# Kernel optimization log

Hardware: AMD Instinct MI355X
Metric: run time of the kernel (lower is better)

Reference implementation:

```python
import math
import jax, jax.numpy as jnp
import numpy as np

B, S, D, L = 8, 4096, 1024, 16

def setup_inputs() -> dict:
    key = jax.random.key(0)
    k1, k2, k3 = jax.random.split(key, 3)
    memory = jax.random.normal(k1, (B, S, D), dtype=jnp.float32)
    summarizer = jax.random.normal(k2, (L, D), dtype=jnp.float32) * 0.02
    w_proj = jax.random.normal(k3, (1, L), dtype=jnp.float32) * (1.0 / math.sqrt(L))
    return {"memory": memory, "summarizer": summarizer, "w_proj": w_proj}

def reference(memory, summarizer, w_proj):
    # scores: [B, L, S] = summarizer @ memory^T / sqrt(D)
    d = summarizer.shape[-1]
    scores = jnp.einsum('ld,bsd->bls', summarizer, memory) / jnp.sqrt(jnp.asarray(d, memory.dtype))
    p_attn = jax.nn.softmax(scores, axis=-1)            # softmax over sequence S
    ctx = jnp.einsum('bls,bsd->bld', p_attn, memory)    # [B, L, D]
    # nn.Linear(L, 1, bias=False) applied to ctx.transpose(-1,-2): [B, D, L] @ W^T -> [B, D, 1]
    out = jnp.einsum('bld,l->bd', ctx, w_proj[0])       # [B, D]
    return out[:, None, :]                              # [B, 1, D] after final transpose
```

## Files before the change

### kernel.cpp

```cpp
#include <hip/hip_runtime.h>
#include <hip/hip_bf16.h>

#define BB 8
#define SS 4096
#define DD 1024
#define LL 16

typedef __attribute__((ext_vector_type(8))) short short8;
typedef __attribute__((ext_vector_type(4))) float fl4;

static __device__ __forceinline__ short f2bf(float f) {
    unsigned u = __float_as_uint(f);
    u += 0x7FFFu + ((u >> 16) & 1u);
    return (short)(u >> 16);
}

__global__ __launch_bounds__(256) void k_prep(const float* __restrict__ summ,
                                              short* __restrict__ summb) {
    int i = blockIdx.x * 256 + threadIdx.x;
    if (i < LL * DD) summb[i] = f2bf(summ[i]);
}

__global__ __launch_bounds__(256) void k_scores(const float* __restrict__ mem,
                                                const short* __restrict__ summb,
                                                float* __restrict__ e) {
    int gwave = (blockIdx.x * 256 + threadIdx.x) >> 6;
    int lane  = threadIdx.x & 63;
    int b     = gwave >> 8;
    int s0    = (gwave & 255) << 4;
    int o  = lane & 15;
    int qd = lane >> 4;

    const short* arow = summb + o * DD + qd * 8;
    const float* mrow = mem + ((size_t)b * SS + (size_t)(s0 + o)) * DD + qd * 8;

    fl4 acc = {0.f, 0.f, 0.f, 0.f};
    #pragma unroll 8
    for (int k = 0; k < DD; k += 32) {
        short8 a = *(const short8*)(arow + k);
        fl4 f0 = *(const fl4*)(mrow + k);
        fl4 f1 = *(const fl4*)(mrow + k + 4);
        short8 bb;
        bb[0] = f2bf(f0[0]); bb[1] = f2bf(f0[1]);
        bb[2] = f2bf(f0[2]); bb[3] = f2bf(f0[3]);
        bb[4] = f2bf(f1[0]); bb[5] = f2bf(f1[1]);
        bb[6] = f2bf(f1[2]); bb[7] = f2bf(f1[3]);
        acc = __builtin_amdgcn_mfma_f32_16x16x32_bf16(a, bb, acc, 0, 0, 0);
    }

    const float scale = 0.03125f;
    float* ebase = e + (size_t)b * LL * SS + s0 + o;
    #pragma unroll
    for (int r = 0; r < 4; ++r) {
        int l = qd * 4 + r;
        ebase[(size_t)l * SS] = __expf(acc[r] * scale);
    }
}

__global__ __launch_bounds__(1024) void k_softmax_q(const float* __restrict__ e,
                                                    const float* __restrict__ w,
                                                    float* __restrict__ qout) {
    int b = blockIdx.x;
    int t = threadIdx.x;
    int l = t >> 6, u = t & 63;
    __shared__ float coef[LL];
    const float* eb = e + (size_t)b * LL * SS;

    float sum = 0.f;
    #pragma unroll 8
    for (int s = u; s < SS; s += 64) sum += eb[(size_t)l * SS + s];
    #pragma unroll
    for (int m = 32; m >= 1; m >>= 1) sum += __shfl_xor(sum, m, 64);
    if (u == 0) coef[l] = w[l] / sum;
    __syncthreads();

    float c[LL];
    #pragma unroll
    for (int i = 0; i < LL; ++i) c[i] = coef[i];
    #pragma unroll
    for (int s = t; s < SS; s += 1024) {
        float qv = 0.f;
        #pragma unroll
        for (int l2 = 0; l2 < LL; ++l2) qv += c[l2] * eb[(size_t)l2 * SS + s];
        qout[(size_t)b * SS + s] = qv;
    }
}

__global__ __launch_bounds__(256) void k_ctx(const float* __restrict__ mem,
                                             const float* __restrict__ qv,
                                             float* __restrict__ out) {
    int blk = blockIdx.x;
    int b  = blk >> 6;
    int ch = blk & 63;
    int t = threadIdx.x;
    int s0 = ch * 64;
    const float* mb = mem + ((size_t)b * SS + s0) * DD + t * 4;
    const float* qb = qv + (size_t)b * SS + s0;

    __shared__ float qs[64];
    if (t < 64) qs[t] = qb[t];
    __syncthreads();

    fl4 acc = {0.f, 0.f, 0.f, 0.f};
    #pragma unroll 8
    for (int i = 0; i < 64; ++i) {
        fl4 m4 = *(const fl4*)(mb + (size_t)i * DD);
        acc += qs[i] * m4;
    }
    float* op = out + (size_t)b * DD + t * 4;
    atomicAdd(op + 0, acc[0]);
    atomicAdd(op + 1, acc[1]);
    atomicAdd(op + 2, acc[2]);
    atomicAdd(op + 3, acc[3]);
}

extern "C" void kernel_launch(void* const* d_in, const int* in_sizes, int n_in,
                              void* d_out, int out_size, void* d_ws, size_t ws_size,
                              hipStream_t stream) {
    const float* mem  = (const float*)d_in[0];
    const float* summ = (const float*)d_in[1];
    const float* w    = (const float*)d_in[2];
    float* out = (float*)d_out;

    char* ws = (char*)d_ws;
    short* summb = (short*)ws;
    float* e     = (float*)(ws + 64 * 1024);
    float* q     = (float*)(ws + 64 * 1024 + 2 * 1024 * 1024);

    hipMemsetAsync(out, 0, (size_t)out_size * sizeof(float), stream);
    k_prep<<<64, 256, 0, stream>>>(summ, summb);
    k_scores<<<(BB * SS / 16) / 4, 256, 0, stream>>>(mem, summb, e);
    k_softmax_q<<<BB, 1024, 0, stream>>>(e, w, q);
    k_ctx<<<BB * 64, 256, 0, stream>>>(mem, q, out);
}
```

Before: 229.3 us.

## Fuse softmax normalization into score and context kernels via atomic partial sums

Removes the separate softmax/q kernel, which ran on only one block per batch. Per-row exponential sums are now reduced inside the score kernel with shuffles and shared memory, then added to a global Z buffer with atomics. The context kernel computes the combined per-position weights from e, Z and w itself. The e layout changes to [b][s][l] so each position's 16 values sit together, and the output memset moves into the prep kernel; the cost is extra atomics and a recomputation of q in every context block.

```diff
diff --git a/kernel.cpp b/kernel.cpp
--- a/kernel.cpp
+++ b/kernel.cpp
@@ -16,15 +16,21 @@
 }
 
 __global__ __launch_bounds__(256) void k_prep(const float* __restrict__ summ,
-                                              short* __restrict__ summb) {
+                                              short* __restrict__ summb,
+                                              float* __restrict__ Z,
+                                              float* __restrict__ out) {
     int i = blockIdx.x * 256 + threadIdx.x;
     if (i < LL * DD) summb[i] = f2bf(summ[i]);
+    if (i < BB * LL) Z[i] = 0.f;
+    if (i < BB * DD) out[i] = 0.f;
 }
 
 __global__ __launch_bounds__(256) void k_scores(const float* __restrict__ mem,
                                                 const short* __restrict__ summb,
-                                                float* __restrict__ e) {
-    int gwave = (blockIdx.x * 256 + threadIdx.x) >> 6;
+                                                float* __restrict__ e,
+                                                float* __restrict__ Z) {
+    int widx  = threadIdx.x >> 6;
+    int gwave = blockIdx.x * 4 + widx;
     int lane  = threadIdx.x & 63;
     int b     = gwave >> 8;
     int s0    = (gwave & 255) << 4;
@@ -49,58 +55,61 @@
     }
 
     const float scale = 0.03125f;
-    float* ebase = e + (size_t)b * LL * SS + s0 + o;
+    float ev[4];
+    float* ebase = e + ((size_t)b * SS + s0) * LL;
     #pragma unroll
     for (int r = 0; r < 4; ++r) {
-        int l = qd * 4 + r;
-        ebase[(size_t)l * SS] = __expf(acc[r] * scale);
+        ev[r] = __expf(acc[r] * scale);
+        ebase[o * LL + qd * 4 + r] = ev[r];
     }
-}
 
-__global__ __launch_bounds__(1024) void k_softmax_q(const float* __restrict__ e,
-                                                    const float* __restrict__ w,
-                                                    float* __restrict__ qout) {
-    int b = blockIdx.x;
+    #pragma unroll
+    for (int r = 0; r < 4; ++r) {
+        float v = ev[r];
+        v += __shfl_xor(v, 1, 64);
+        v += __shfl_xor(v, 2, 64);
+        v += __shfl_xor(v, 4, 64);
+        v += __shfl_xor(v, 8, 64);
+        ev[r] = v;
+    }
+    __shared__ float zp[4][LL];
+    if (o == 0) {
+        #pragma unroll
+        for (int r = 0; r < 4; ++r) zp[widx][qd * 4 + r] = ev[r];
+    }
+    __syncthreads();
     int t = threadIdx.x;
-    int l = t >> 6, u = t & 63;
-    __shared__ float coef[LL];
-    const float* eb = e + (size_t)b * LL * SS;
-
-    float sum = 0.f;
-    #pragma unroll 8
-    for (int s = u; s < SS; s += 64) sum += eb[(size_t)l * SS + s];
-    #pragma unroll
-    for (int m = 32; m >= 1; m >>= 1) sum += __shfl_xor(sum, m, 64);
-    if (u == 0) coef[l] = w[l] / sum;
-    __syncthreads();
-
-    float c[LL];
-    #pragma unroll
-    for (int i = 0; i < LL; ++i) c[i] = coef[i];
-    #pragma unroll
-    for (int s = t; s < SS; s += 1024) {
-        float qv = 0.f;
-        #pragma unroll
-        for (int l2 = 0; l2 < LL; ++l2) qv += c[l2] * eb[(size_t)l2 * SS + s];
-        qout[(size_t)b * SS + s] = qv;
+    if (t < LL) {
+        float v = zp[0][t] + zp[1][t] + zp[2][t] + zp[3][t];
+        atomicAdd(&Z[b * LL + t], v);
     }
 }
 
 __global__ __launch_bounds__(256) void k_ctx(const float* __restrict__ mem,
-                                             const float* __restrict__ qv,
+                                             const float* __restrict__ e,
+                                             const float* __restrict__ Z,
+                                             const float* __restrict__ w,
                                              float* __restrict__ out) {
     int blk = blockIdx.x;
     int b  = blk >> 6;
     int ch = blk & 63;
     int t = threadIdx.x;
     int s0 = ch * 64;
-    const float* mb = mem + ((size_t)b * SS + s0) * DD + t * 4;
-    const float* qb = qv + (size_t)b * SS + s0;
 
+    __shared__ float coef[LL];
     __shared__ float qs[64];
-    if (t < 64) qs[t] = qb[t];
+    if (t < LL) coef[t] = w[t] / Z[b * LL + t];
+    __syncthreads();
+    if (t < 64) {
+        const float* ep = e + ((size_t)b * SS + s0 + t) * LL;
+        float qv = 0.f;
+        #pragma unroll
+        for (int l = 0; l < LL; ++l) qv += coef[l] * ep[l];
+        qs[t] = qv;
+    }
     __syncthreads();
 
+    const float* mb = mem + ((size_t)b * SS + s0) * DD + t * 4;
     fl4 acc = {0.f, 0.f, 0.f, 0.f};
     #pragma unroll 8
     for (int i = 0; i < 64; ++i) {
@@ -124,12 +133,10 @@
 
     char* ws = (char*)d_ws;
     short* summb = (short*)ws;
-    float* e     = (float*)(ws + 64 * 1024);
-    float* q     = (float*)(ws + 64 * 1024 + 2 * 1024 * 1024);
+    float* Z     = (float*)(ws + 64 * 1024);
+    float* e     = (float*)(ws + 68 * 1024);
 
-    hipMemsetAsync(out, 0, (size_t)out_size * sizeof(float), stream);
-    k_prep<<<64, 256, 0, stream>>>(summ, summb);
-    k_scores<<<(BB * SS / 16) / 4, 256, 0, stream>>>(mem, summb, e);
-    k_softmax_q<<<BB, 1024, 0, stream>>>(e, w, q);
-    k_ctx<<<BB * 64, 256, 0, stream>>>(mem, q, out);
+    k_prep<<<64, 256, 0, stream>>>(summ, summb, Z, out);
+    k_scores<<<(BB * SS / 16) / 4, 256, 0, stream>>>(mem, summb, e, Z);
+    k_ctx<<<BB * 64, 256, 0, stream>>>(mem, e, Z, w, out);
 }
```

Result: faster. 219.7 us (-4.2%).
